# Kernel optimization log

Measured on AMD Instinct MI355X. Metric: run time of the kernel, lower is better.

The kernel has to match this reference:

```python
import jax, jax.numpy as jnp
import numpy as np

EPS = 1e-6

def setup_inputs() -> dict:
    key = jax.random.key(0)
    ks = jax.random.split(key, 6)
    B, C, T, H, W = 4, 512, 32, 32, 32
    x = jax.random.normal(ks[0], (B, C, T, H, W), dtype=jnp.float32)
    gamma = jnp.ones((C,), dtype=jnp.float32)
    beta = jnp.zeros((C,), dtype=jnp.float32)
    s = 1.0 / np.sqrt(C)
    wq = jax.random.normal(ks[1], (C, C), dtype=jnp.float32) * s
    wk = jax.random.normal(ks[2], (C, C), dtype=jnp.float32) * s
    wv = jax.random.normal(ks[3], (C, C), dtype=jnp.float32) * s
    wproj = jax.random.normal(ks[4], (C, C), dtype=jnp.float32) * s
    return {"x": x, "gamma": gamma, "beta": beta, "wq": wq, "wk": wk, "wv": wv, "wproj": wproj}

def reference(x, gamma, beta, wq, wk, wv, wproj):
    B, C, T, H, W = x.shape
    # CausalGroupNorm(num_groups=1): per-(B,T) frame LayerNorm over (C,H,W)
    mean = jnp.mean(x, axis=(1, 3, 4), keepdims=True)
    var = jnp.var(x, axis=(1, 3, 4), keepdims=True)
    h = (x - mean) * jax.lax.rsqrt(var + EPS)
    h = h * gamma[None, :, None, None, None] + beta[None, :, None, None, None]
    # per-pixel temporal sequences: [B*H*W, C, T]
    h = h.transpose(0, 3, 4, 1, 2).reshape(B * H * W, C, T)
    q = jnp.einsum('oc,bct->bot', wq, h)
    k = jnp.einsum('oc,bct->bot', wk, h)
    v = jnp.einsum('oc,bct->bot', wv, h)
    scale = C ** (-0.5)
    attn = jnp.einsum('bct,bcs->bts', q, k) * scale  # [BHW, T, T]
    causal = jnp.tril(jnp.ones((T, T), dtype=bool))
    attn = jnp.where(causal[None], attn, -jnp.inf)
    attn = jax.nn.softmax(attn, axis=-1)
    out = jnp.einsum('bts,bcs->bct', attn, v)
    out = jnp.einsum('oc,bct->bot', wproj, out)
    out = out.reshape(B, H, W, C, T).transpose(0, 3, 4, 1, 2)
    return x + out
```

## Files before the change

### kernel.cpp

```cpp
#include <hip/hip_runtime.h>
#include <hip/hip_bf16.h>

typedef __attribute__((ext_vector_type(4))) float f32x4;
typedef __attribute__((ext_vector_type(8))) short bf16x8;
typedef __attribute__((ext_vector_type(4))) int   i32x4;
typedef __attribute__((ext_vector_type(2))) int   i32x2;

#define HT0 0u
#define GT0 65536u
#define PT0 131072u
#define LG0 135168u
#define K3_LDS 143360
#define QK_SCALE 0.04419417382415922f

static __device__ __forceinline__ unsigned short f2bf(float f) {
    unsigned int u = __builtin_bit_cast(unsigned int, f);
    u += 0x7fffu + ((u >> 16) & 1u);
    return (unsigned short)(u >> 16);
}
static __device__ __forceinline__ float bf2f(unsigned short h) {
    unsigned int u = ((unsigned int)h) << 16;
    return __builtin_bit_cast(float, u);
}
static __device__ __forceinline__ f32x4 fzero() {
    f32x4 v; v[0] = 0.f; v[1] = 0.f; v[2] = 0.f; v[3] = 0.f; return v;
}

__global__ __launch_bounds__(256) void kw_weights(
    const float* __restrict__ wq, const float* __restrict__ wk,
    const float* __restrict__ wproj, const float* __restrict__ wv,
    unsigned short* __restrict__ wqk, unsigned short* __restrict__ wpv)
{
    int bx = blockIdx.x;
    int mat = bx >> 6;
    int tile = bx & 63;
    int i0 = (tile >> 3) * 64, j0 = (tile & 7) * 64;
    const float* A  = mat ? wproj : wq;
    const float* Bm = mat ? wv : wk;
    unsigned short* Out = mat ? wpv : wqk;
    __shared__ float At[16][64];
    __shared__ float Bt[16][64];
    int tid = threadIdx.x;
    int ty = tid >> 4, tx = tid & 15;
    float acc[4][4] = {};
    for (int k0 = 0; k0 < 512; k0 += 16) {
        if (mat == 0) {
#pragma unroll
            for (int r = 0; r < 4; ++r) {
                int idx = r * 256 + tid;
                At[idx >> 6][idx & 63] = A[(size_t)(k0 + (idx >> 6)) * 512 + i0 + (idx & 63)];
            }
        } else {
#pragma unroll
            for (int r = 0; r < 4; ++r) {
                int idx = r * 256 + tid;
                At[idx & 15][idx >> 4] = A[(size_t)(i0 + (idx >> 4)) * 512 + k0 + (idx & 15)];
            }
        }
#pragma unroll
        for (int r = 0; r < 4; ++r) {
            int idx = r * 256 + tid;
            Bt[idx >> 6][idx & 63] = Bm[(size_t)(k0 + (idx >> 6)) * 512 + j0 + (idx & 63)];
        }
        __syncthreads();
#pragma unroll
        for (int kk = 0; kk < 16; ++kk)
#pragma unroll
            for (int i = 0; i < 4; ++i)
#pragma unroll
                for (int j = 0; j < 4; ++j)
                    acc[i][j] += At[kk][ty * 4 + i] * Bt[kk][tx * 4 + j];
        __syncthreads();
    }
#pragma unroll
    for (int i = 0; i < 4; ++i) {
        ushort4 o;
        o.x = f2bf(acc[i][0]); o.y = f2bf(acc[i][1]);
        o.z = f2bf(acc[i][2]); o.w = f2bf(acc[i][3]);
        *(ushort4*)(Out + (size_t)(i0 + ty * 4 + i) * 512 + j0 + tx * 4) = o;
    }
}

__global__ __launch_bounds__(512) void k_transpose_stats(
    const float* __restrict__ x, unsigned short* __restrict__ Hraw, float* __restrict__ sums)
{
    int bx = blockIdx.x;
    int tp = bx & 15;
    int h  = (bx >> 4) & 31;
    int bb = bx >> 9;
    int t0 = tp * 2;
    int tid = threadIdx.x;
    extern __shared__ char lds[];
    float* red = (float*)(lds + 65536);

    int tt = (tid >> 3) & 1;
    int w4 = tid & 7;
    int cb = tid >> 4;
    float s = 0.f, q = 0.f;
    const unsigned int Kt = (unsigned int)tt * 64u + (unsigned int)w4 * 8u;
#pragma unroll
    for (int it = 0; it < 16; ++it) {
        int c = it * 32 + cb;
        float4 v = *(const float4*)(x + (((size_t)(bb * 512 + c)) * 32 + (t0 + tt)) * 1024 + h * 32 + w4 * 4);
        s += v.x + v.y + v.z + v.w;
        q += v.x * v.x + v.y * v.y + v.z * v.z + v.w * v.w;
        unsigned int p0 = ((unsigned int)f2bf(v.y) << 16) | f2bf(v.x);
        unsigned int p1 = ((unsigned int)f2bf(v.w) << 16) | f2bf(v.z);
        unsigned int Kx = ((unsigned int)((c >> 3) & 31)) << 2;
        unsigned int base = (unsigned int)c * 128u + Kt;
        *(unsigned int*)(lds + ((base + 0u) ^ Kx)) = p0;
        *(unsigned int*)(lds + ((base + 4u) ^ Kx)) = p1;
    }
    s += __shfl_xor(s, 1);  q += __shfl_xor(q, 1);
    s += __shfl_xor(s, 2);  q += __shfl_xor(q, 2);
    s += __shfl_xor(s, 4);  q += __shfl_xor(q, 4);
    s += __shfl_xor(s, 16); q += __shfl_xor(q, 16);
    s += __shfl_xor(s, 32); q += __shfl_xor(q, 32);
    int wid = tid >> 6, lane = tid & 63;
    if (lane == 0) { red[wid * 4 + 0] = s; red[wid * 4 + 1] = q; }
    if (lane == 8) { red[wid * 4 + 2] = s; red[wid * 4 + 3] = q; }
    __syncthreads();
    if (tid < 4) {
        float a = 0.f;
#pragma unroll
        for (int w = 0; w < 8; ++w) a += red[w * 4 + tid];
        int f = bb * 32 + t0 + (tid >> 1);
        atomicAdd(&sums[f * 2 + (tid & 1)], a);
    }
#pragma unroll
    for (int rnd = 0; rnd < 8; ++rnd) {
        int row = rnd * 8 + wid;
        int w = row >> 1, ttw = row & 1;
        int c0 = lane * 8;
        unsigned short e[8];
#pragma unroll
        for (int j = 0; j < 8; ++j) {
            int c = c0 + j;
            unsigned int Kx = ((unsigned int)((c >> 3) & 31)) << 2;
            unsigned int off = ((unsigned int)(c * 128 + ttw * 64 + 2 * w)) ^ Kx;
            e[j] = *(const unsigned short*)(lds + off);
        }
        i32x4 ov;
        ov[0] = (int)(((unsigned int)e[1] << 16) | e[0]);
        ov[1] = (int)(((unsigned int)e[3] << 16) | e[2]);
        ov[2] = (int)(((unsigned int)e[5] << 16) | e[4]);
        ov[3] = (int)(((unsigned int)e[7] << 16) | e[6]);
        size_t pix = ((size_t)bb * 32 + h) * 32 + w;
        *(i32x4*)(Hraw + pix * 16384 + (size_t)(t0 + ttw) * 512 + c0) = ov;
    }
}

__global__ void k_finalize(const float* __restrict__ sums, float* __restrict__ mr) {
    int f = threadIdx.x;
    float mean = sums[f * 2] * (1.f / 524288.f);
    float var  = sums[f * 2 + 1] * (1.f / 524288.f) - mean * mean;
    mr[f * 2]     = mean;
    mr[f * 2 + 1] = rsqrtf(var + 1e-6f);
}

static __device__ __forceinline__ void mfma16(f32x4 (&acc)[4][4], const bf16x8 (&a)[4], const bf16x8 (&b)[4]) {
#pragma unroll
    for (int mt = 0; mt < 4; ++mt)
#pragma unroll
        for (int nf = 0; nf < 4; ++nf)
            acc[mt][nf] = __builtin_amdgcn_mfma_f32_16x16x32_bf16(a[mt], b[nf], acc[mt][nf], 0, 0, 0);
}
static __device__ __forceinline__ void load_w4(bf16x8 (&a)[4], const unsigned short* wbase, int k0) {
#pragma unroll
    for (int mt = 0; mt < 4; ++mt)
        a[mt] = *(const bf16x8*)(wbase + (size_t)mt * 16 * 512 + k0);
}
static __device__ __forceinline__ void load_h4(bf16x8 (&b)[4], const char* ldsb, int lo, int hi, int k0) {
#pragma unroll
    for (int nf = 0; nf < 4; ++nf) {
        int row = nf * 16 + lo;
        unsigned off = ((unsigned)(row * 1024 + (k0 + hi * 8) * 2)) ^ (((unsigned)(row & 7)) << 4);
        b[nf] = *(const bf16x8*)(ldsb + off);
    }
}

__global__ __launch_bounds__(512, 2) void k_attn(
    const unsigned short* Hraw,
    const unsigned short* __restrict__ Wqk,
    const unsigned short* __restrict__ Wpv,
    const float* __restrict__ gamma, const float* __restrict__ beta,
    const float* __restrict__ mr,
    unsigned short* OA)
{
    extern __shared__ char lds[];
    int tid = threadIdx.x, wid = tid >> 6, lane = tid & 63;
    int lo = lane & 15, hi = lane >> 4;
    int pix0 = blockIdx.x * 2;
    int b_ = pix0 >> 10;

    {
        const unsigned short* src = Hraw + (size_t)pix0 * 16384;
#pragma unroll
        for (int it = 0; it < 8; ++it) {
            int chunk = it * 512 + tid;
            int row = chunk >> 6;
            int col = chunk & 63;
            int t = row & 31;
            float2 mrv = *(const float2*)(mr + ((b_ << 5) + t) * 2);
            i32x4 v = *(const i32x4*)(src + (size_t)chunk * 8);
            int c0 = col * 8;
            float4 g0 = *(const float4*)(gamma + c0);
            float4 g1 = *(const float4*)(gamma + c0 + 4);
            float4 be0 = *(const float4*)(beta + c0);
            float4 be1 = *(const float4*)(beta + c0 + 4);
            float mu = mrv.x, rs = mrv.y;
            i32x4 ov;
            {
                float xa = bf2f((unsigned short)(v[0] & 0xffff));
                float xb = bf2f((unsigned short)((unsigned int)v[0] >> 16));
                ov[0] = (int)((((unsigned int)f2bf((xb - mu) * (rs * g0.y) + be0.y)) << 16) | f2bf((xa - mu) * (rs * g0.x) + be0.x));
            }
            {
                float xa = bf2f((unsigned short)(v[1] & 0xffff));
                float xb = bf2f((unsigned short)((unsigned int)v[1] >> 16));
                ov[1] = (int)((((unsigned int)f2bf((xb - mu) * (rs * g0.w) + be0.w)) << 16) | f2bf((xa - mu) * (rs * g0.z) + be0.z));
            }
            {
                float xa = bf2f((unsigned short)(v[2] & 0xffff));
                float xb = bf2f((unsigned short)((unsigned int)v[2] >> 16));
                ov[2] = (int)((((unsigned int)f2bf((xb - mu) * (rs * g1.y) + be1.y)) << 16) | f2bf((xa - mu) * (rs * g1.x) + be1.x));
            }
            {
                float xa = bf2f((unsigned short)(v[3] & 0xffff));
                float xb = bf2f((unsigned short)((unsigned int)v[3] >> 16));
                ov[3] = (int)((((unsigned int)f2bf((xb - mu) * (rs * g1.w) + be1.w)) << 16) | f2bf((xa - mu) * (rs * g1.z) + be1.z));
            }
            unsigned off = ((unsigned)(row * 1024 + col * 16)) ^ (((unsigned)(row & 7)) << 4);
            *(i32x4*)(lds + HT0 + off) = ov;
        }
    }
    __syncthreads();

    {
        f32x4 acc[4][4];
#pragma unroll
        for (int mt = 0; mt < 4; ++mt)
#pragma unroll
            for (int nf = 0; nf < 4; ++nf) acc[mt][nf] = fzero();
        const unsigned short* wbase = Wqk + (size_t)(wid * 64 + lo) * 512 + hi * 8;
        bf16x8 a0[4], b0v[4], a1[4], b1v[4];
        load_w4(a0, wbase, 0);
        load_h4(b0v, lds + HT0, lo, hi, 0);
#pragma unroll 2
        for (int kk = 0; kk < 8; ++kk) {
            int k0 = kk * 64;
            load_w4(a1, wbase, k0 + 32);
            load_h4(b1v, lds + HT0, lo, hi, k0 + 32);
            mfma16(acc, a0, b0v);
            if (kk < 7) {
                load_w4(a0, wbase, k0 + 64);
                load_h4(b0v, lds + HT0, lo, hi, k0 + 64);
            }
            mfma16(acc, a1, b1v);
        }
#pragma unroll
        for (int mt = 0; mt < 4; ++mt)
#pragma unroll
            for (int nf = 0; nf < 4; ++nf) {
                int n = nf * 16 + lo;
                int c0 = wid * 64 + mt * 16 + hi * 4;
                unsigned int w0 = ((unsigned int)f2bf(acc[mt][nf][1]) << 16) | f2bf(acc[mt][nf][0]);
                unsigned int w1 = ((unsigned int)f2bf(acc[mt][nf][3]) << 16) | f2bf(acc[mt][nf][2]);
                unsigned off = ((unsigned)(n * 1024 + c0 * 2)) ^ (((unsigned)(n & 7)) << 4);
                i32x2 pv; pv[0] = (int)w0; pv[1] = (int)w1;
                *(i32x2*)(lds + GT0 + off) = pv;
            }
    }
    __syncthreads();

    {
        int p = wid >> 2, tth = (wid >> 1) & 1, sh = wid & 1;
        int arow = p * 32 + tth * 16 + lo;
        int brow = p * 32 + sh * 16 + lo;
        f32x4 acc = fzero();
#pragma unroll 4
        for (int k0 = 0; k0 < 512; k0 += 32) {
            unsigned aoff = ((unsigned)(arow * 1024 + (k0 + hi * 8) * 2)) ^ (((unsigned)(arow & 7)) << 4);
            unsigned boff = ((unsigned)(brow * 1024 + (k0 + hi * 8) * 2)) ^ (((unsigned)(brow & 7)) << 4);
            bf16x8 a = *(const bf16x8*)(lds + HT0 + aoff);
            bf16x8 b = *(const bf16x8*)(lds + GT0 + boff);
            acc = __builtin_amdgcn_mfma_f32_16x16x32_bf16(a, b, acc, 0, 0, 0);
        }
#pragma unroll
        for (int r = 0; r < 4; ++r) {
            int t = tth * 16 + hi * 4 + r;
            int s = sh * 16 + lo;
            *(float*)(lds + LG0 + (unsigned)(((p * 32 + t) * 32 + s) * 4)) = acc[r] * QK_SCALE;
        }
    }
    __syncthreads();

    {
        int row = tid >> 3;
        int p = row >> 5, t = row & 31;
        int s0 = (tid & 7) * 4;
        f32x4 v = *(const f32x4*)(lds + LG0 + (unsigned)(((p * 32 + t) * 32 + s0) * 4));
        float vv0 = (s0 + 0 <= t) ? v[0] : -1e30f;
        float vv1 = (s0 + 1 <= t) ? v[1] : -1e30f;
        float vv2 = (s0 + 2 <= t) ? v[2] : -1e30f;
        float vv3 = (s0 + 3 <= t) ? v[3] : -1e30f;
        float m = fmaxf(fmaxf(vv0, vv1), fmaxf(vv2, vv3));
        m = fmaxf(m, __shfl_xor(m, 1));
        m = fmaxf(m, __shfl_xor(m, 2));
        m = fmaxf(m, __shfl_xor(m, 4));
        float e0 = __expf(vv0 - m), e1 = __expf(vv1 - m), e2 = __expf(vv2 - m), e3 = __expf(vv3 - m);
        float sum = e0 + e1 + e2 + e3;
        sum += __shfl_xor(sum, 1);
        sum += __shfl_xor(sum, 2);
        sum += __shfl_xor(sum, 4);
        float inv = 1.0f / sum;
        unsigned int w0 = ((unsigned int)f2bf(e1 * inv) << 16) | f2bf(e0 * inv);
        unsigned int w1 = ((unsigned int)f2bf(e3 * inv) << 16) | f2bf(e2 * inv);
        unsigned off = ((unsigned)((p * 32 + t) * 64 + s0 * 2)) ^ (((unsigned)(t & 3)) << 4);
        i32x2 pv; pv[0] = (int)w0; pv[1] = (int)w1;
        *(i32x2*)(lds + PT0 + off) = pv;
    }
    __syncthreads();

    {
        f32x4 acc[4][4];
#pragma unroll
        for (int mt = 0; mt < 4; ++mt)
#pragma unroll
            for (int of = 0; of < 4; ++of) acc[mt][of] = fzero();
        const unsigned short* wbase = Wpv + (size_t)(wid * 64 + lo) * 512 + hi * 8;
        bf16x8 a0[4], b0v[4], a1[4], b1v[4];
        load_h4(a0, lds + HT0, lo, hi, 0);
        load_w4(b0v, wbase, 0);
#pragma unroll 2
        for (int kk = 0; kk < 8; ++kk) {
            int k0 = kk * 64;
            load_h4(a1, lds + HT0, lo, hi, k0 + 32);
            load_w4(b1v, wbase, k0 + 32);
            mfma16(acc, a0, b0v);
            if (kk < 7) {
                load_h4(a0, lds + HT0, lo, hi, k0 + 64);
                load_w4(b0v, wbase, k0 + 64);
            }
            mfma16(acc, a1, b1v);
        }
#pragma unroll
        for (int mt = 0; mt < 4; ++mt)
#pragma unroll
            for (int of = 0; of < 4; ++of) {
                int o = wid * 64 + of * 16 + lo;
                int n0 = mt * 16 + hi * 4;
                unsigned int w0 = ((unsigned int)f2bf(acc[mt][of][1]) << 16) | f2bf(acc[mt][of][0]);
                unsigned int w1 = ((unsigned int)f2bf(acc[mt][of][3]) << 16) | f2bf(acc[mt][of][2]);
                unsigned off = ((unsigned)(o * 128 + n0 * 2)) ^ (((unsigned)(o & 7)) << 4);
                i32x2 pv; pv[0] = (int)w0; pv[1] = (int)w1;
                *(i32x2*)(lds + GT0 + off) = pv;
            }
    }
    __syncthreads();

    {
        f32x4 oacc[4][4];
#pragma unroll
        for (int rt = 0; rt < 4; ++rt) {
            int p = rt >> 1;
            int ar = rt * 16 + lo;
            unsigned aoff = ((unsigned)(ar * 64 + hi * 16)) ^ (((unsigned)(ar & 3)) << 4);
            bf16x8 a = *(const bf16x8*)(lds + PT0 + aoff);
#pragma unroll
            for (int of = 0; of < 4; ++of) {
                int o = wid * 64 + of * 16 + lo;
                unsigned boff = ((unsigned)(o * 128 + (p * 32 + hi * 8) * 2)) ^ (((unsigned)(o & 7)) << 4);
                bf16x8 b = *(const bf16x8*)(lds + GT0 + boff);
                oacc[rt][of] = __builtin_amdgcn_mfma_f32_16x16x32_bf16(a, b, fzero(), 0, 0, 0);
            }
        }
        unsigned otb = HT0 + (unsigned)wid * 8192u;
#pragma unroll
        for (int rt = 0; rt < 4; ++rt)
#pragma unroll
            for (int of = 0; of < 4; ++of) {
                int oc = of * 16 + lo;
                int n0 = rt * 16 + hi * 4;
                unsigned int w0 = ((unsigned int)f2bf(oacc[rt][of][1]) << 16) | f2bf(oacc[rt][of][0]);
                unsigned int w1 = ((unsigned int)f2bf(oacc[rt][of][3]) << 16) | f2bf(oacc[rt][of][2]);
                unsigned off = ((unsigned)(oc * 128 + n0 * 2)) ^ (((unsigned)(oc & 7)) << 4);
                i32x2 pv; pv[0] = (int)w0; pv[1] = (int)w1;
                *(i32x2*)(lds + otb + off) = pv;
            }
        int p_ = lane >> 5, ohi = (lane >> 2) & 7, tq = lane & 3;
        size_t pixg = (size_t)(pix0 + p_);
#pragma unroll
        for (int i = 0; i < 8; ++i) {
            int o = i * 8 + ohi;
            unsigned off = ((unsigned)(o * 128 + (p_ * 32 + tq * 8) * 2)) ^ (((unsigned)(o & 7)) << 4);
            i32x4 v = *(const i32x4*)(lds + otb + off);
            *(i32x4*)(OA + pixg * 16384 + (size_t)(wid * 64 + o) * 32 + tq * 8) = v;
        }
    }
}

__global__ __launch_bounds__(512) void k_output(
    const float* __restrict__ x, const unsigned short* __restrict__ OA, float* __restrict__ out)
{
    int bx = blockIdx.x;
    int cbk = bx & 31;
    int h = (bx >> 5) & 31;
    int bb = bx >> 10;
    int c0 = cbk * 16;
    int tid = threadIdx.x;
    extern __shared__ char lds[];

#pragma unroll
    for (int it = 0; it < 4; ++it) {
        int chunk = it * 512 + tid;
        int pix = chunk >> 6;
        int rem = chunk & 63;
        int c = rem >> 2;
        int th = rem & 3;
        size_t pixg = ((size_t)bb * 32 + h) * 32 + pix;
        i32x4 v = *(const i32x4*)(OA + pixg * 16384 + (size_t)(c0 + c) * 32 + th * 8);
        unsigned Kx = ((unsigned)(pix & 31)) << 2;
        unsigned base = (unsigned)(pix * 1024 + c * 64 + th * 16);
        *(unsigned int*)(lds + ((base + 0u) ^ Kx))  = (unsigned int)v[0];
        *(unsigned int*)(lds + ((base + 4u) ^ Kx))  = (unsigned int)v[1];
        *(unsigned int*)(lds + ((base + 8u) ^ Kx))  = (unsigned int)v[2];
        *(unsigned int*)(lds + ((base + 12u) ^ Kx)) = (unsigned int)v[3];
    }
    __syncthreads();
#pragma unroll
    for (int it = 0; it < 8; ++it) {
        int flat4 = it * 512 + tid;
        int c = flat4 >> 8;
        int rem = flat4 & 255;
        int t = rem >> 3, w4 = rem & 7;
        size_t gidx = (((size_t)(bb * 512 + c0 + c)) * 32 + t) * 1024 + h * 32 + w4 * 4;
        float4 xv = *(const float4*)(x + gidx);
        float4 ov;
        {
            int pix = w4 * 4 + 0;
            unsigned off = ((unsigned)(pix * 1024 + c * 64 + t * 2)) ^ (((unsigned)(pix & 31)) << 2);
            ov.x = xv.x + bf2f(*(const unsigned short*)(lds + off));
        }
        {
            int pix = w4 * 4 + 1;
            unsigned off = ((unsigned)(pix * 1024 + c * 64 + t * 2)) ^ (((unsigned)(pix & 31)) << 2);
            ov.y = xv.y + bf2f(*(const unsigned short*)(lds + off));
        }
        {
            int pix = w4 * 4 + 2;
            unsigned off = ((unsigned)(pix * 1024 + c * 64 + t * 2)) ^ (((unsigned)(pix & 31)) << 2);
            ov.z = xv.z + bf2f(*(const unsigned short*)(lds + off));
        }
        {
            int pix = w4 * 4 + 3;
            unsigned off = ((unsigned)(pix * 1024 + c * 64 + t * 2)) ^ (((unsigned)(pix & 31)) << 2);
            ov.w = xv.w + bf2f(*(const unsigned short*)(lds + off));
        }
        *(float4*)(out + gidx) = ov;
    }
}

extern "C" void kernel_launch(void* const* d_in, const int* in_sizes, int n_in,
                              void* d_out, int out_size, void* d_ws, size_t ws_size,
                              hipStream_t stream)
{
    const float* x     = (const float*)d_in[0];
    const float* gamma = (const float*)d_in[1];
    const float* beta  = (const float*)d_in[2];
    const float* wq    = (const float*)d_in[3];
    const float* wk    = (const float*)d_in[4];
    const float* wv    = (const float*)d_in[5];
    const float* wproj = (const float*)d_in[6];
    float* out = (float*)d_out;

    char* ws = (char*)d_ws;
    unsigned short* Hbuf = (unsigned short*)ws;
    unsigned short* Wqk  = (unsigned short*)(ws + 134217728);
    unsigned short* Wpv  = (unsigned short*)(ws + 134217728 + 524288);
    float* sums = (float*)(ws + 134217728 + 1048576);
    float* mr   = (float*)(ws + 134217728 + 1048576 + 1024);

    hipMemsetAsync(sums, 0, 256 * sizeof(float), stream);

    hipFuncSetAttribute((const void*)k_transpose_stats, hipFuncAttributeMaxDynamicSharedMemorySize, 65536 + 128);
    hipFuncSetAttribute((const void*)k_attn, hipFuncAttributeMaxDynamicSharedMemorySize, K3_LDS);

    kw_weights<<<dim3(128), dim3(256), 0, stream>>>(wq, wk, wproj, wv, Wqk, Wpv);
    k_transpose_stats<<<dim3(2048), dim3(512), 65536 + 128, stream>>>(x, Hbuf, sums);
    k_finalize<<<dim3(1), dim3(128), 0, stream>>>(sums, mr);
    k_attn<<<dim3(2048), dim3(512), K3_LDS, stream>>>(Hbuf, Wqk, Wpv, gamma, beta, mr, Hbuf);
    k_output<<<dim3(4096), dim3(512), 32768, stream>>>(x, Hbuf, out);
}
```

Before: 572.9 us.

## Process one pixel per attention block to halve LDS and raise occupancy

The attention kernel now handles one pixel per workgroup instead of two. That shrinks LDS from about 140KB to about 74KB, halves the accumulator register tiles, and raises the occupancy hint from 2 to 4 blocks. The QK^T step splits the K dimension across wave pairs and sums the partial logits in the softmax stage. The softmax syncthreads before the PV GEMM is removed, since that GEMM does not read P. The cost is that each weight tile is reused across only 32 columns instead of 64, which doubles global/L2 weight traffic per pixel, and only half the threads work in the softmax.

```diff
diff --git a/kernel.cpp b/kernel.cpp
--- a/kernel.cpp
+++ b/kernel.cpp
@@ -7,10 +7,10 @@
 typedef __attribute__((ext_vector_type(2))) int   i32x2;
 
 #define HT0 0u
-#define GT0 65536u
-#define PT0 131072u
-#define LG0 135168u
-#define K3_LDS 143360
+#define GT0 32768u
+#define LG0 65536u
+#define PT0 73728u
+#define K3_LDS 75776
 #define QK_SCALE 0.04419417382415922f
 
 static __device__ __forceinline__ unsigned short f2bf(float f) {
@@ -158,28 +158,21 @@
     mr[f * 2 + 1] = rsqrtf(var + 1e-6f);
 }
 
-static __device__ __forceinline__ void mfma16(f32x4 (&acc)[4][4], const bf16x8 (&a)[4], const bf16x8 (&b)[4]) {
-#pragma unroll
-    for (int mt = 0; mt < 4; ++mt)
-#pragma unroll
-        for (int nf = 0; nf < 4; ++nf)
-            acc[mt][nf] = __builtin_amdgcn_mfma_f32_16x16x32_bf16(a[mt], b[nf], acc[mt][nf], 0, 0, 0);
-}
 static __device__ __forceinline__ void load_w4(bf16x8 (&a)[4], const unsigned short* wbase, int k0) {
 #pragma unroll
     for (int mt = 0; mt < 4; ++mt)
         a[mt] = *(const bf16x8*)(wbase + (size_t)mt * 16 * 512 + k0);
 }
-static __device__ __forceinline__ void load_h4(bf16x8 (&b)[4], const char* ldsb, int lo, int hi, int k0) {
-#pragma unroll
-    for (int nf = 0; nf < 4; ++nf) {
+static __device__ __forceinline__ void load_h2(bf16x8 (&b)[2], const char* ldsb, int lo, int hi, int k0) {
+#pragma unroll
+    for (int nf = 0; nf < 2; ++nf) {
         int row = nf * 16 + lo;
         unsigned off = ((unsigned)(row * 1024 + (k0 + hi * 8) * 2)) ^ (((unsigned)(row & 7)) << 4);
         b[nf] = *(const bf16x8*)(ldsb + off);
     }
 }
 
-__global__ __launch_bounds__(512, 2) void k_attn(
+__global__ __launch_bounds__(512, 4) void k_attn(
     const unsigned short* Hraw,
     const unsigned short* __restrict__ Wqk,
     const unsigned short* __restrict__ Wpv,
@@ -190,18 +183,17 @@
     extern __shared__ char lds[];
     int tid = threadIdx.x, wid = tid >> 6, lane = tid & 63;
     int lo = lane & 15, hi = lane >> 4;
-    int pix0 = blockIdx.x * 2;
-    int b_ = pix0 >> 10;
+    int pix = blockIdx.x;
+    int b_ = pix >> 10;
 
     {
-        const unsigned short* src = Hraw + (size_t)pix0 * 16384;
-#pragma unroll
-        for (int it = 0; it < 8; ++it) {
+        const unsigned short* src = Hraw + (size_t)pix * 16384;
+#pragma unroll
+        for (int it = 0; it < 4; ++it) {
             int chunk = it * 512 + tid;
             int row = chunk >> 6;
             int col = chunk & 63;
-            int t = row & 31;
-            float2 mrv = *(const float2*)(mr + ((b_ << 5) + t) * 2);
+            float2 mrv = *(const float2*)(mr + ((b_ << 5) + row) * 2);
             i32x4 v = *(const i32x4*)(src + (size_t)chunk * 8);
             int c0 = col * 8;
             float4 g0 = *(const float4*)(gamma + c0);
@@ -237,31 +229,39 @@
     __syncthreads();
 
     {
-        f32x4 acc[4][4];
+        f32x4 acc[4][2];
 #pragma unroll
         for (int mt = 0; mt < 4; ++mt)
 #pragma unroll
-            for (int nf = 0; nf < 4; ++nf) acc[mt][nf] = fzero();
+            for (int nf = 0; nf < 2; ++nf) acc[mt][nf] = fzero();
         const unsigned short* wbase = Wqk + (size_t)(wid * 64 + lo) * 512 + hi * 8;
-        bf16x8 a0[4], b0v[4], a1[4], b1v[4];
+        bf16x8 a0[4], a1[4], b0[2], b1[2];
         load_w4(a0, wbase, 0);
-        load_h4(b0v, lds + HT0, lo, hi, 0);
+        load_h2(b0, lds + HT0, lo, hi, 0);
 #pragma unroll 2
         for (int kk = 0; kk < 8; ++kk) {
             int k0 = kk * 64;
             load_w4(a1, wbase, k0 + 32);
-            load_h4(b1v, lds + HT0, lo, hi, k0 + 32);
-            mfma16(acc, a0, b0v);
+            load_h2(b1, lds + HT0, lo, hi, k0 + 32);
+#pragma unroll
+            for (int mt = 0; mt < 4; ++mt)
+#pragma unroll
+                for (int nf = 0; nf < 2; ++nf)
+                    acc[mt][nf] = __builtin_amdgcn_mfma_f32_16x16x32_bf16(a0[mt], b0[nf], acc[mt][nf], 0, 0, 0);
             if (kk < 7) {
                 load_w4(a0, wbase, k0 + 64);
-                load_h4(b0v, lds + HT0, lo, hi, k0 + 64);
-            }
-            mfma16(acc, a1, b1v);
+                load_h2(b0, lds + HT0, lo, hi, k0 + 64);
+            }
+#pragma unroll
+            for (int mt = 0; mt < 4; ++mt)
+#pragma unroll
+                for (int nf = 0; nf < 2; ++nf)
+                    acc[mt][nf] = __builtin_amdgcn_mfma_f32_16x16x32_bf16(a1[mt], b1[nf], acc[mt][nf], 0, 0, 0);
         }
 #pragma unroll
         for (int mt = 0; mt < 4; ++mt)
 #pragma unroll
-            for (int nf = 0; nf < 4; ++nf) {
+            for (int nf = 0; nf < 2; ++nf) {
                 int n = nf * 16 + lo;
                 int c0 = wid * 64 + mt * 16 + hi * 4;
                 unsigned int w0 = ((unsigned int)f2bf(acc[mt][nf][1]) << 16) | f2bf(acc[mt][nf][0]);
@@ -274,12 +274,13 @@
     __syncthreads();
 
     {
-        int p = wid >> 2, tth = (wid >> 1) & 1, sh = wid & 1;
-        int arow = p * 32 + tth * 16 + lo;
-        int brow = p * 32 + sh * 16 + lo;
+        int kh = wid & 1, sh = (wid >> 1) & 1, th = wid >> 2;
+        int arow = th * 16 + lo;
+        int brow = sh * 16 + lo;
         f32x4 acc = fzero();
-#pragma unroll 4
-        for (int k0 = 0; k0 < 512; k0 += 32) {
+#pragma unroll
+        for (int j = 0; j < 8; ++j) {
+            int k0 = kh * 256 + j * 32;
             unsigned aoff = ((unsigned)(arow * 1024 + (k0 + hi * 8) * 2)) ^ (((unsigned)(arow & 7)) << 4);
             unsigned boff = ((unsigned)(brow * 1024 + (k0 + hi * 8) * 2)) ^ (((unsigned)(brow & 7)) << 4);
             bf16x8 a = *(const bf16x8*)(lds + HT0 + aoff);
@@ -288,22 +289,22 @@
         }
 #pragma unroll
         for (int r = 0; r < 4; ++r) {
-            int t = tth * 16 + hi * 4 + r;
+            int t = th * 16 + hi * 4 + r;
             int s = sh * 16 + lo;
-            *(float*)(lds + LG0 + (unsigned)(((p * 32 + t) * 32 + s) * 4)) = acc[r] * QK_SCALE;
-        }
-    }
-    __syncthreads();
-
-    {
-        int row = tid >> 3;
-        int p = row >> 5, t = row & 31;
+            *(float*)(lds + LG0 + (unsigned)(kh * 4096 + (t * 32 + s) * 4)) = acc[r];
+        }
+    }
+    __syncthreads();
+
+    if (tid < 256) {
+        int t = tid >> 3;
         int s0 = (tid & 7) * 4;
-        f32x4 v = *(const f32x4*)(lds + LG0 + (unsigned)(((p * 32 + t) * 32 + s0) * 4));
-        float vv0 = (s0 + 0 <= t) ? v[0] : -1e30f;
-        float vv1 = (s0 + 1 <= t) ? v[1] : -1e30f;
-        float vv2 = (s0 + 2 <= t) ? v[2] : -1e30f;
-        float vv3 = (s0 + 3 <= t) ? v[3] : -1e30f;
+        f32x4 v0 = *(const f32x4*)(lds + LG0 + (unsigned)((t * 32 + s0) * 4));
+        f32x4 v1 = *(const f32x4*)(lds + LG0 + (unsigned)(4096 + (t * 32 + s0) * 4));
+        float vv0 = (s0 + 0 <= t) ? (v0[0] + v1[0]) * QK_SCALE : -1e30f;
+        float vv1 = (s0 + 1 <= t) ? (v0[1] + v1[1]) * QK_SCALE : -1e30f;
+        float vv2 = (s0 + 2 <= t) ? (v0[2] + v1[2]) * QK_SCALE : -1e30f;
+        float vv3 = (s0 + 3 <= t) ? (v0[3] + v1[3]) * QK_SCALE : -1e30f;
         float m = fmaxf(fmaxf(vv0, vv1), fmaxf(vv2, vv3));
         m = fmaxf(m, __shfl_xor(m, 1));
         m = fmaxf(m, __shfl_xor(m, 2));
@@ -316,43 +317,49 @@
         float inv = 1.0f / sum;
         unsigned int w0 = ((unsigned int)f2bf(e1 * inv) << 16) | f2bf(e0 * inv);
         unsigned int w1 = ((unsigned int)f2bf(e3 * inv) << 16) | f2bf(e2 * inv);
-        unsigned off = ((unsigned)((p * 32 + t) * 64 + s0 * 2)) ^ (((unsigned)(t & 3)) << 4);
+        unsigned off = ((unsigned)(t * 64 + s0 * 2)) ^ (((unsigned)(t & 3)) << 4);
         i32x2 pv; pv[0] = (int)w0; pv[1] = (int)w1;
         *(i32x2*)(lds + PT0 + off) = pv;
     }
-    __syncthreads();
-
     {
-        f32x4 acc[4][4];
-#pragma unroll
-        for (int mt = 0; mt < 4; ++mt)
+        f32x4 acc[2][4];
+#pragma unroll
+        for (int mt = 0; mt < 2; ++mt)
 #pragma unroll
             for (int of = 0; of < 4; ++of) acc[mt][of] = fzero();
         const unsigned short* wbase = Wpv + (size_t)(wid * 64 + lo) * 512 + hi * 8;
-        bf16x8 a0[4], b0v[4], a1[4], b1v[4];
-        load_h4(a0, lds + HT0, lo, hi, 0);
-        load_w4(b0v, wbase, 0);
+        bf16x8 a0[2], a1[2], b0[4], b1[4];
+        load_h2(a0, lds + HT0, lo, hi, 0);
+        load_w4(b0, wbase, 0);
 #pragma unroll 2
         for (int kk = 0; kk < 8; ++kk) {
             int k0 = kk * 64;
-            load_h4(a1, lds + HT0, lo, hi, k0 + 32);
-            load_w4(b1v, wbase, k0 + 32);
-            mfma16(acc, a0, b0v);
+            load_h2(a1, lds + HT0, lo, hi, k0 + 32);
+            load_w4(b1, wbase, k0 + 32);
+#pragma unroll
+            for (int mt = 0; mt < 2; ++mt)
+#pragma unroll
+                for (int of = 0; of < 4; ++of)
+                    acc[mt][of] = __builtin_amdgcn_mfma_f32_16x16x32_bf16(a0[mt], b0[of], acc[mt][of], 0, 0, 0);
             if (kk < 7) {
-                load_h4(a0, lds + HT0, lo, hi, k0 + 64);
-                load_w4(b0v, wbase, k0 + 64);
-            }
-            mfma16(acc, a1, b1v);
-        }
-#pragma unroll
-        for (int mt = 0; mt < 4; ++mt)
+                load_h2(a0, lds + HT0, lo, hi, k0 + 64);
+                load_w4(b0, wbase, k0 + 64);
+            }
+#pragma unroll
+            for (int mt = 0; mt < 2; ++mt)
+#pragma unroll
+                for (int of = 0; of < 4; ++of)
+                    acc[mt][of] = __builtin_amdgcn_mfma_f32_16x16x32_bf16(a1[mt], b1[of], acc[mt][of], 0, 0, 0);
+        }
+#pragma unroll
+        for (int mt = 0; mt < 2; ++mt)
 #pragma unroll
             for (int of = 0; of < 4; ++of) {
                 int o = wid * 64 + of * 16 + lo;
                 int n0 = mt * 16 + hi * 4;
                 unsigned int w0 = ((unsigned int)f2bf(acc[mt][of][1]) << 16) | f2bf(acc[mt][of][0]);
                 unsigned int w1 = ((unsigned int)f2bf(acc[mt][of][3]) << 16) | f2bf(acc[mt][of][2]);
-                unsigned off = ((unsigned)(o * 128 + n0 * 2)) ^ (((unsigned)(o & 7)) << 4);
+                unsigned off = ((unsigned)(o * 64 + n0 * 2)) ^ (((unsigned)(o & 3)) << 4);
                 i32x2 pv; pv[0] = (int)w0; pv[1] = (int)w1;
                 *(i32x2*)(lds + GT0 + off) = pv;
             }
@@ -360,42 +367,39 @@
     __syncthreads();
 
     {
-        f32x4 oacc[4][4];
-#pragma unroll
-        for (int rt = 0; rt < 4; ++rt) {
-            int p = rt >> 1;
-            int ar = rt * 16 + lo;
-            unsigned aoff = ((unsigned)(ar * 64 + hi * 16)) ^ (((unsigned)(ar & 3)) << 4);
+        f32x4 accF[2][4];
+#pragma unroll
+        for (int tt = 0; tt < 2; ++tt) {
+            int arow = tt * 16 + lo;
+            unsigned aoff = ((unsigned)(arow * 64 + hi * 16)) ^ (((unsigned)(arow & 3)) << 4);
             bf16x8 a = *(const bf16x8*)(lds + PT0 + aoff);
 #pragma unroll
             for (int of = 0; of < 4; ++of) {
                 int o = wid * 64 + of * 16 + lo;
-                unsigned boff = ((unsigned)(o * 128 + (p * 32 + hi * 8) * 2)) ^ (((unsigned)(o & 7)) << 4);
+                unsigned boff = ((unsigned)(o * 64 + hi * 16)) ^ (((unsigned)(o & 3)) << 4);
                 bf16x8 b = *(const bf16x8*)(lds + GT0 + boff);
-                oacc[rt][of] = __builtin_amdgcn_mfma_f32_16x16x32_bf16(a, b, fzero(), 0, 0, 0);
-            }
-        }
-        unsigned otb = HT0 + (unsigned)wid * 8192u;
-#pragma unroll
-        for (int rt = 0; rt < 4; ++rt)
+                accF[tt][of] = __builtin_amdgcn_mfma_f32_16x16x32_bf16(a, b, fzero(), 0, 0, 0);
+            }
+        }
+#pragma unroll
+        for (int tt = 0; tt < 2; ++tt)
 #pragma unroll
             for (int of = 0; of < 4; ++of) {
-                int oc = of * 16 + lo;
-                int n0 = rt * 16 + hi * 4;
-                unsigned int w0 = ((unsigned int)f2bf(oacc[rt][of][1]) << 16) | f2bf(oacc[rt][of][0]);
-                unsigned int w1 = ((unsigned int)f2bf(oacc[rt][of][3]) << 16) | f2bf(oacc[rt][of][2]);
-                unsigned off = ((unsigned)(oc * 128 + n0 * 2)) ^ (((unsigned)(oc & 7)) << 4);
+                int o = wid * 64 + of * 16 + lo;
+                int t0 = tt * 16 + hi * 4;
+                unsigned int w0 = ((unsigned int)f2bf(accF[tt][of][1]) << 16) | f2bf(accF[tt][of][0]);
+                unsigned int w1 = ((unsigned int)f2bf(accF[tt][of][3]) << 16) | f2bf(accF[tt][of][2]);
+                unsigned off = ((unsigned)(o * 64 + t0 * 2)) ^ (((unsigned)(o & 3)) << 4);
                 i32x2 pv; pv[0] = (int)w0; pv[1] = (int)w1;
-                *(i32x2*)(lds + otb + off) = pv;
-            }
-        int p_ = lane >> 5, ohi = (lane >> 2) & 7, tq = lane & 3;
-        size_t pixg = (size_t)(pix0 + p_);
-#pragma unroll
-        for (int i = 0; i < 8; ++i) {
-            int o = i * 8 + ohi;
-            unsigned off = ((unsigned)(o * 128 + (p_ * 32 + tq * 8) * 2)) ^ (((unsigned)(o & 7)) << 4);
-            i32x4 v = *(const i32x4*)(lds + otb + off);
-            *(i32x4*)(OA + pixg * 16384 + (size_t)(wid * 64 + o) * 32 + tq * 8) = v;
+                *(i32x2*)(lds + HT0 + off) = pv;
+            }
+        int or_ = lane >> 2, tq = lane & 3;
+#pragma unroll
+        for (int i = 0; i < 4; ++i) {
+            int o = wid * 64 + i * 16 + or_;
+            unsigned off = ((unsigned)(o * 64 + tq * 16)) ^ (((unsigned)(o & 3)) << 4);
+            i32x4 v = *(const i32x4*)(lds + HT0 + off);
+            *(i32x4*)(OA + (size_t)pix * 16384 + (size_t)o * 32 + tq * 8) = v;
         }
     }
 }
@@ -489,6 +493,6 @@
     kw_weights<<<dim3(128), dim3(256), 0, stream>>>(wq, wk, wproj, wv, Wqk, Wpv);
     k_transpose_stats<<<dim3(2048), dim3(512), 65536 + 128, stream>>>(x, Hbuf, sums);
     k_finalize<<<dim3(1), dim3(128), 0, stream>>>(sums, mr);
-    k_attn<<<dim3(2048), dim3(512), K3_LDS, stream>>>(Hbuf, Wqk, Wpv, gamma, beta, mr, Hbuf);
+    k_attn<<<dim3(4096), dim3(512), K3_LDS, stream>>>(Hbuf, Wqk, Wpv, gamma, beta, mr, Hbuf);
     k_output<<<dim3(4096), dim3(512), 32768, stream>>>(x, Hbuf, out);
 }
```

New measurement: 742.8 us (median of 3 runs). 1.3x slower.
